# Kernel optimization log

Measured on AMD Instinct MI355X. Metric: run time of the kernel, lower is better.

The kernel has to match this reference:

```python
import jax, jax.numpy as jnp
import numpy as np

N_NODES = 200000
N_EDGES = 6400000
N_GRAPHS = 1024
N_EMB = 1032
D = 16


def _gcn_conv(x, W, b, src, dst, n):
    # PyG GCNConv: h = x W; symmetric norm with self-loops; aggregate onto target (dst)
    h = x @ W
    deg = jax.ops.segment_sum(jnp.ones_like(dst, dtype=h.dtype), dst, num_segments=n) + 1.0
    dis = jax.lax.rsqrt(deg)
    norm = dis[src] * dis[dst]                      # [E]
    agg = jax.ops.segment_sum(h[src] * norm[:, None], dst, num_segments=n)
    agg = agg + h * (dis * dis)[:, None]            # self-loop term
    return agg + b


def _protein_embed(ids, edge_index, batch_ids, emb, W1, b1, W2, b2):
    n = ids.shape[0]
    x = emb[ids]                                    # embedding lookup [N, D]
    src, dst = edge_index[0], edge_index[1]
    h = jax.nn.relu(_gcn_conv(x, W1, b1, src, dst, n))
    h = _gcn_conv(h, W2, b2, src, dst, n)
    # global_mean_pool over graphs
    sums = jax.ops.segment_sum(h, batch_ids, num_segments=N_GRAPHS)
    cnt = jax.ops.segment_sum(jnp.ones((n,), h.dtype), batch_ids, num_segments=N_GRAPHS)
    return sums / jnp.maximum(cnt, 1.0)[:, None]    # [B, D]


def setup_inputs() -> dict:
    key = jax.random.key(0)
    ks = jax.random.split(key, 10)
    emb = jax.random.normal(ks[0], (N_EMB, D), jnp.float32) * 0.1
    W1 = jax.random.normal(ks[1], (D, D), jnp.float32) * (1.0 / np.sqrt(D))
    W2 = jax.random.normal(ks[2], (D, D), jnp.float32) * (1.0 / np.sqrt(D))
    fcW = jax.random.normal(ks[3], (6, 2 * D), jnp.float32) * (1.0 / np.sqrt(2 * D))
    b1 = jnp.zeros((D,), jnp.float32)
    b2 = jnp.zeros((D,), jnp.float32)
    fcb = jnp.zeros((6,), jnp.float32)
    rx = jax.random.randint(ks[4], (N_NODES,), 0, N_EMB)
    r_edge_index = jax.random.randint(ks[5], (2, N_EDGES), 0, N_NODES)
    r_batch = jnp.sort(jax.random.randint(ks[6], (N_NODES,), 0, N_GRAPHS))
    lx = jax.random.randint(ks[7], (N_NODES,), 0, N_EMB)
    l_edge_index = jax.random.randint(ks[8], (2, N_EDGES), 0, N_NODES)
    l_batch = jnp.sort(jax.random.randint(ks[9], (N_NODES,), 0, N_GRAPHS))
    return {"emb": emb, "W1": W1, "b1": b1, "W2": W2, "b2": b2, "fcW": fcW, "fcb": fcb,
            "rx": rx, "r_edge_index": r_edge_index, "r_batch": r_batch,
            "lx": lx, "l_edge_index": l_edge_index, "l_batch": l_batch}


def reference(emb, W1, b1, W2, b2, fcW, fcb, rx, r_edge_index, r_batch, lx, l_edge_index, l_batch):
    r = _protein_embed(rx, r_edge_index, r_batch, emb, W1, b1, W2, b2)
    l = _protein_embed(lx, l_edge_index, l_batch, emb, W1, b1, W2, b2)
    h = jnp.concatenate([r, l], axis=1)             # [B, 2D]
    out = h @ fcW.T + fcb                           # [B, 6]
    return out[:, :3], out[:, 3:]
```

## Files before the change

kernel.cpp:

```cpp
#include <hip/hip_runtime.h>
#include <hip/hip_bf16.h>

#define N_NODES 200000
#define N_GRAPHS 1024
#define D 16
#define NEDGE 6400000

#define BNODES 256
#define NBUK 782
#define NCH 512
#define ECHUNK 12500
#define OSTRIDE (NBUK + 1)
#define CAP 9216
#define GBLK 12500
#define GHALF 6250

__global__ __launch_bounds__(1024) void pA(
        const int* __restrict__ srcR, const int* __restrict__ dstR,
        const int* __restrict__ srcL, const int* __restrict__ dstL,
        unsigned int* __restrict__ slabC_R, unsigned int* __restrict__ slabC_L,
        int* __restrict__ offsT_R, int* __restrict__ offsT_L) {
    const int* src = blockIdx.y ? srcL : srcR;
    const int* dst = blockIdx.y ? dstL : dstR;
    unsigned int* slabC = blockIdx.y ? slabC_L : slabC_R;
    int* offsT = blockIdx.y ? offsT_L : offsT_R;

    __shared__ unsigned int stage[ECHUNK];
    __shared__ int lh[NBUK];
    __shared__ int lcur[NBUK];
    __shared__ int wsum[16];
    int t = threadIdx.x;
    int wave = t >> 6, lane = t & 63;
    int c = blockIdx.x;
    int base = c * ECHUNK;

    for (int k = t; k < NBUK; k += 1024) lh[k] = 0;
    __syncthreads();
    for (int e = t; e < ECHUNK; e += 1024)
        atomicAdd(&lh[((unsigned int)dst[base + e]) >> 8], 1);
    __syncthreads();

    int v = (t < NBUK) ? lh[t] : 0;
    int x = v;
#pragma unroll
    for (int d0 = 1; d0 < 64; d0 <<= 1) {
        int y = __shfl_up(x, d0, 64);
        if (lane >= d0) x += y;
    }
    if (lane == 63) wsum[wave] = x;
    __syncthreads();
    if (wave == 0 && lane < 16) {
        int s = wsum[lane];
#pragma unroll
        for (int d0 = 1; d0 < 16; d0 <<= 1) {
            int y = __shfl_up(s, d0, 64);
            if (lane >= d0) s += y;
        }
        wsum[lane] = s;
    }
    __syncthreads();
    int excl = x - v + (wave ? wsum[wave - 1] : 0);
    if (t < NBUK) lcur[t] = excl;
    __syncthreads();

    for (int e = t; e < ECHUNK; e += 1024) {
        int d = dst[base + e];
        int s = src[base + e];
        int pos = atomicAdd(&lcur[d >> 8], 1);
        stage[pos] = ((unsigned int)(d & 255) << 18) | (unsigned int)s;
    }
    __syncthreads();
    for (int e = t; e < ECHUNK; e += 1024) slabC[base + e] = stage[e];
    if (t < NBUK) offsT[c * OSTRIDE + t] = excl;
    if (t == 0) offsT[c * OSTRIDE + NBUK] = ECHUNK;
}

__global__ __launch_bounds__(256) void tr_kernel(
        const int* __restrict__ offsT_R, const int* __restrict__ offsT_L,
        int* __restrict__ offsTT_R, int* __restrict__ offsTT_L) {
    const int* in = blockIdx.z ? offsT_L : offsT_R;
    int* outp = blockIdx.z ? offsTT_L : offsTT_R;
    __shared__ int tile[32][33];
    int lx = threadIdx.x & 31, ly = threadIdx.x >> 5;
#pragma unroll
    for (int r = 0; r < 32; r += 8) {
        int row = blockIdx.y * 32 + ly + r;
        int col = blockIdx.x * 32 + lx;
        if (col < OSTRIDE) tile[ly + r][lx] = in[row * OSTRIDE + col];
    }
    __syncthreads();
#pragma unroll
    for (int r = 0; r < 32; r += 8) {
        int orow = blockIdx.x * 32 + ly + r;
        int ocol = blockIdx.y * 32 + lx;
        if (orow < OSTRIDE) outp[orow * NCH + ocol] = tile[lx][ly + r];
    }
}

__global__ __launch_bounds__(256) void pB(
        const unsigned int* __restrict__ slabC_R, const unsigned int* __restrict__ slabC_L,
        const int* __restrict__ offsTT_R, const int* __restrict__ offsTT_L,
        unsigned int* __restrict__ slabR, unsigned int* __restrict__ slabL,
        int2* __restrict__ metaR, int2* __restrict__ metaL,
        float* __restrict__ disR, float* __restrict__ disL) {
    int y = blockIdx.y;
    const unsigned int* slabC = y ? slabC_L : slabC_R;
    const int* offsTT = y ? offsTT_L : offsTT_R;
    unsigned int* slab = y ? slabL : slabR;
    int2* meta = y ? metaL : metaR;
    float* dis = y ? disL : disR;

    __shared__ unsigned int sin_[CAP];
    __shared__ unsigned int sout[CAP];
    __shared__ int hcnt[BNODES], hoff[BNODES], hcur[BNODES];
    __shared__ int wtot[4];
    __shared__ int totc;
    int t = threadIdx.x;
    int lane = t & 63, wave = t >> 6;
    int b = blockIdx.x;

    int a0 = offsTT[b * NCH + t],        e0 = offsTT[(b + 1) * NCH + t];
    int a1 = offsTT[b * NCH + t + 256],  e1 = offsTT[(b + 1) * NCH + t + 256];
    int len = (e0 - a0) + (e1 - a1);

    int x = len;
#pragma unroll
    for (int d0 = 1; d0 < 64; d0 <<= 1) {
        int yy = __shfl_up(x, d0, 64);
        if (lane >= d0) x += yy;
    }
    if (lane == 63) wtot[wave] = x;
    hcnt[t] = 0;
    __syncthreads();
    int pre = 0;
    for (int w2 = 0; w2 < wave; w2++) pre += wtot[w2];
    int sbase = x - len + pre;
    if (t == 255) totc = sbase + len;
    __syncthreads();

    int p = sbase;
    {
        int cb = t * ECHUNK;
        for (int i = (a0 & ~3); i < e0; i += 4) {
            uint4 v = *(const uint4*)(slabC + cb + i);
            unsigned int vv[4] = {v.x, v.y, v.z, v.w};
#pragma unroll
            for (int k = 0; k < 4; k++) {
                int idx = i + k;
                if (idx >= a0 && idx < e0) { if (p < CAP) sin_[p] = vv[k]; p++; }
            }
        }
        cb = (t + 256) * ECHUNK;
        for (int i = (a1 & ~3); i < e1; i += 4) {
            uint4 v = *(const uint4*)(slabC + cb + i);
            unsigned int vv[4] = {v.x, v.y, v.z, v.w};
#pragma unroll
            for (int k = 0; k < 4; k++) {
                int idx = i + k;
                if (idx >= a1 && idx < e1) { if (p < CAP) sin_[p] = vv[k]; p++; }
            }
        }
    }
    __syncthreads();
    int cnt = totc;
    if (cnt > CAP) cnt = CAP;

    for (int i = t; i < cnt; i += 256) atomicAdd(&hcnt[sin_[i] >> 18], 1);
    __syncthreads();

    int v2 = hcnt[t];
    int x2 = v2;
#pragma unroll
    for (int d0 = 1; d0 < 64; d0 <<= 1) {
        int yy = __shfl_up(x2, d0, 64);
        if (lane >= d0) x2 += yy;
    }
    if (lane == 63) wtot[wave] = x2;
    __syncthreads();
    int pre2 = 0;
    for (int w2 = 0; w2 < wave; w2++) pre2 += wtot[w2];
    int ex = x2 - v2 + pre2;
    hoff[t] = ex;
    hcur[t] = ex;
    __syncthreads();

    for (int i = t; i < cnt; i += 256) {
        unsigned int r = sin_[i];
        int pp = atomicAdd(&hcur[r >> 18], 1);
        if (pp < CAP) sout[pp] = r & 0x3FFFFu;
    }
    __syncthreads();

    int gb = b * CAP;
    for (int i = t; i < cnt; i += 256) slab[gb + i] = sout[i];
    int node = (b << 8) + t;
    if (node < N_NODES) {
        meta[node] = make_int2(gb + hoff[t], gb + hoff[t] + hcnt[t]);
        dis[node] = rsqrtf((float)hcnt[t] + 1.0f);
    }
}

__global__ __launch_bounds__(256) void t1_kernel(
        const int* __restrict__ idsR, const int* __restrict__ idsL,
        const float* __restrict__ emb, const float* __restrict__ W,
        const float* __restrict__ disR, const float* __restrict__ disL,
        __hip_bfloat16* __restrict__ hsR, __hip_bfloat16* __restrict__ hsL) {
    int y = blockIdx.y;
    const int* ids = y ? idsL : idsR;
    const float* dis = y ? disL : disR;
    __hip_bfloat16* hs = y ? hsL : hsR;
    __shared__ float sW[D][D];
    __shared__ float sx[16][D + 1];
    int t = threadIdx.x;
    int j = t & 15, g = t >> 4;
    sW[g][j] = W[t];
    int i = (blockIdx.x << 4) + g;
    sx[g][j] = emb[(size_t)ids[i] * D + j];
    __syncthreads();
    float acc = 0.f;
#pragma unroll
    for (int k = 0; k < D; k++) acc += sx[g][k] * sW[k][j];
    hs[(size_t)i * D + j] = __float2bfloat16(acc * dis[i]);
}

__global__ __launch_bounds__(256) void g1_kernel(
        const int2* __restrict__ metaR, const int2* __restrict__ metaL,
        const unsigned int* __restrict__ csrR, const unsigned int* __restrict__ csrL,
        const __hip_bfloat16* __restrict__ hs1R, const __hip_bfloat16* __restrict__ hs1L,
        const float* __restrict__ disR, const float* __restrict__ disL,
        const float* __restrict__ b1, const float* __restrict__ W2,
        __hip_bfloat16* __restrict__ hs2R, __hip_bfloat16* __restrict__ hs2L) {
    int half = (blockIdx.x >= GHALF);
    int bx = blockIdx.x - (half ? GHALF : 0);
    const int2* meta = half ? metaL : metaR;
    const unsigned int* csr = half ? csrL : csrR;
    const __hip_bfloat16* hs1 = half ? hs1L : hs1R;
    const float* dis = half ? disL : disR;
    __hip_bfloat16* hs2 = half ? hs2L : hs2R;

    __shared__ float sW[D][D];
    __shared__ float sx[32][D + 1];
    int t = threadIdx.x;
    int jp = t & 7, g = t >> 3;
    sW[t >> 4][t & 15] = W2[t];
    int i = (bx << 5) + g;
    int2 be = meta[i];
    float2 acc = __bfloat1622float2(
        *(const __hip_bfloat162*)(hs1 + (size_t)i * D + 2 * jp));
    int e = be.x, end = be.y;
    for (; e + 8 <= end; e += 8) {
        int my = (int)csr[e + jp];
#pragma unroll
        for (int n = 0; n < 8; n++) {
            int s = __shfl(my, n, 8);
            float2 f = __bfloat1622float2(
                *(const __hip_bfloat162*)(hs1 + (size_t)s * D + 2 * jp));
            acc.x += f.x; acc.y += f.y;
        }
    }
    for (; e < end; e++) {
        int s = csr[e];
        float2 f = __bfloat1622float2(
            *(const __hip_bfloat162*)(hs1 + (size_t)s * D + 2 * jp));
        acc.x += f.x; acc.y += f.y;
    }
    float di = dis[i];
    sx[g][2 * jp]     = fmaxf(acc.x * di + b1[2 * jp], 0.f);
    sx[g][2 * jp + 1] = fmaxf(acc.y * di + b1[2 * jp + 1], 0.f);
    __syncthreads();
    float a0 = 0.f, a1 = 0.f;
#pragma unroll
    for (int k = 0; k < D; k++) {
        float xv = sx[g][k];
        a0 += xv * sW[k][2 * jp];
        a1 += xv * sW[k][2 * jp + 1];
    }
    *(__hip_bfloat162*)(hs2 + (size_t)i * D + 2 * jp) =
        __float22bfloat162_rn(make_float2(a0 * di, a1 * di));
}

__global__ __launch_bounds__(256) void g2_kernel(
        const int2* __restrict__ metaR, const int2* __restrict__ metaL,
        const unsigned int* __restrict__ csrR, const unsigned int* __restrict__ csrL,
        const __hip_bfloat16* __restrict__ hs2R, const __hip_bfloat16* __restrict__ hs2L,
        const float* __restrict__ disR, const float* __restrict__ disL,
        const float* __restrict__ b2,
        const int* __restrict__ batR, const int* __restrict__ batL,
        float* __restrict__ sumsR, float* __restrict__ sumsL,
        float* __restrict__ cntR, float* __restrict__ cntL) {
    int half = (blockIdx.x >= GHALF);
    int bx = blockIdx.x - (half ? GHALF : 0);
    const int2* meta = half ? metaL : metaR;
    const unsigned int* csr = half ? csrL : csrR;
    const __hip_bfloat16* hs2 = half ? hs2L : hs2R;
    const float* dis = half ? disL : disR;
    const int* batch = half ? batL : batR;
    float* sums = half ? sumsL : sumsR;
    float* cnt = half ? cntL : cntR;

    __shared__ float sv[32][D + 1];
    __shared__ int sb[32];
    int t = threadIdx.x;
    int jp = t & 7, g = t >> 3;
    int i = (bx << 5) + g;
    int2 be = meta[i];
    float2 acc = __bfloat1622float2(
        *(const __hip_bfloat162*)(hs2 + (size_t)i * D + 2 * jp));
    int e = be.x, end = be.y;
    for (; e + 8 <= end; e += 8) {
        int my = (int)csr[e + jp];
#pragma unroll
        for (int n = 0; n < 8; n++) {
            int s = __shfl(my, n, 8);
            float2 f = __bfloat1622float2(
                *(const __hip_bfloat162*)(hs2 + (size_t)s * D + 2 * jp));
            acc.x += f.x; acc.y += f.y;
        }
    }
    for (; e < end; e++) {
        int s = csr[e];
        float2 f = __bfloat1622float2(
            *(const __hip_bfloat162*)(hs2 + (size_t)s * D + 2 * jp));
        acc.x += f.x; acc.y += f.y;
    }
    float di = dis[i];
    int bi = batch[i];
    sv[g][2 * jp]     = acc.x * di + b2[2 * jp];
    sv[g][2 * jp + 1] = acc.y * di + b2[2 * jp + 1];
    if (jp == 0) sb[g] = bi;
    __syncthreads();
    bool runend = (g == 31) || (sb[g + 1] != bi);
    if (runend) {
        float s0 = 0.f, s1 = 0.f;
        int gg = g;
        while (gg >= 0 && sb[gg] == bi) { s0 += sv[gg][2 * jp]; s1 += sv[gg][2 * jp + 1]; gg--; }
        atomicAdd(&sums[bi * D + 2 * jp], s0);
        atomicAdd(&sums[bi * D + 2 * jp + 1], s1);
        if (jp == 0) atomicAdd(&cnt[bi], (float)(g - gg));
    }
}

__global__ void final_kernel(const float* __restrict__ rs, const float* __restrict__ rc,
                             const float* __restrict__ ls, const float* __restrict__ lc,
                             const float* __restrict__ fcW, const float* __restrict__ fcb,
                             float* __restrict__ out) {
    int b = blockIdx.x * blockDim.x + threadIdx.x;
    if (b >= N_GRAPHS) return;
    float hc[2 * D];
    float rn = fmaxf(rc[b], 1.f), ln = fmaxf(lc[b], 1.f);
#pragma unroll
    for (int j = 0; j < D; j++) {
        hc[j]     = rs[b * D + j] / rn;
        hc[D + j] = ls[b * D + j] / ln;
    }
#pragma unroll
    for (int c = 0; c < 6; c++) {
        float acc = fcb[c];
#pragma unroll
        for (int j = 0; j < 2 * D; j++) acc += hc[j] * fcW[c * 2 * D + j];
        if (c < 3) out[b * 3 + c] = acc;
        else       out[N_GRAPHS * 3 + b * 3 + (c - 3)] = acc;
    }
}

extern "C" void kernel_launch(void* const* d_in, const int* in_sizes, int n_in,
                              void* d_out, int out_size, void* d_ws, size_t ws_size,
                              hipStream_t stream) {
    const float* emb = (const float*)d_in[0];
    const float* W1  = (const float*)d_in[1];
    const float* b1  = (const float*)d_in[2];
    const float* W2  = (const float*)d_in[3];
    const float* b2  = (const float*)d_in[4];
    const float* fcW = (const float*)d_in[5];
    const float* fcb = (const float*)d_in[6];
    const int* rx = (const int*)d_in[7];
    const int* re = (const int*)d_in[8];
    const int* rb = (const int*)d_in[9];
    const int* lx = (const int*)d_in[10];
    const int* le = (const int*)d_in[11];
    const int* lb = (const int*)d_in[12];
    float* out = (float*)d_out;

    char* w = (char*)d_ws;
    unsigned int* slabC_R = (unsigned int*)w;
    __hip_bfloat16* hs1R = (__hip_bfloat16*)w;
    __hip_bfloat16* hs1L = hs1R + (size_t)N_NODES * D;
    __hip_bfloat16* hs2R = hs1L + (size_t)N_NODES * D;
    __hip_bfloat16* hs2L = hs2R + (size_t)N_NODES * D;
    w += (size_t)NEDGE * 4;
    unsigned int* slabC_L = (unsigned int*)w;  w += (size_t)NEDGE * 4;
    unsigned int* slabR = (unsigned int*)w;    w += (size_t)NBUK * CAP * 4;
    unsigned int* slabL = (unsigned int*)w;    w += (size_t)NBUK * CAP * 4;
    int* offsT_R = (int*)w;                    w += (size_t)NCH * OSTRIDE * 4;
    int* offsT_L = (int*)w;                    w += (size_t)NCH * OSTRIDE * 4;
    int* offsTT_R = (int*)w;                   w += (size_t)OSTRIDE * NCH * 4;
    int* offsTT_L = (int*)w;                   w += (size_t)OSTRIDE * NCH * 4;
    int2* metaR = (int2*)w;                    w += (size_t)N_NODES * 8;
    int2* metaL = (int2*)w;                    w += (size_t)N_NODES * 8;
    float* disR = (float*)w;                   w += (size_t)N_NODES * 4;
    float* disL = (float*)w;                   w += (size_t)N_NODES * 4;
    float* sums0 = (float*)w;                  w += (size_t)N_GRAPHS * D * 4;
    float* cnt0  = (float*)w;                  w += (size_t)N_GRAPHS * 4;
    float* sums1 = (float*)w;                  w += (size_t)N_GRAPHS * D * 4;
    float* cnt1  = (float*)w;                  w += (size_t)N_GRAPHS * 4;

    const int* srcR = re;  const int* dstR = re + NEDGE;
    const int* srcL = le;  const int* dstL = le + NEDGE;

    hipMemsetAsync(sums0, 0, ((size_t)N_GRAPHS * (D + 1)) * 2 * sizeof(float), stream);

    pA<<<dim3(NCH, 2), 1024, 0, stream>>>(srcR, dstR, srcL, dstL,
                                          slabC_R, slabC_L, offsT_R, offsT_L);
    tr_kernel<<<dim3((OSTRIDE + 31) / 32, NCH / 32, 2), 256, 0, stream>>>(
        offsT_R, offsT_L, offsTT_R, offsTT_L);
    pB<<<dim3(NBUK, 2), 256, 0, stream>>>(slabC_R, slabC_L, offsTT_R, offsTT_L,
                                          slabR, slabL, metaR, metaL, disR, disL);

    t1_kernel<<<dim3(GBLK, 2), 256, 0, stream>>>(rx, lx, emb, W1, disR, disL, hs1R, hs1L);
    g1_kernel<<<2 * GHALF, 256, 0, stream>>>(metaR, metaL, slabR, slabL,
                                             hs1R, hs1L, disR, disL, b1, W2, hs2R, hs2L);
    g2_kernel<<<2 * GHALF, 256, 0, stream>>>(metaR, metaL, slabR, slabL,
                                             hs2R, hs2L, disR, disL, b2, rb, lb,
                                             sums0, sums1, cnt0, cnt1);
    final_kernel<<<(N_GRAPHS + 255) / 256, 256, 0, stream>>>(
        sums0, cnt0, sums1, cnt1, fcW, fcb, out);
}
```

Baseline: 534.7 us.

## Split node features into two 8-wide planes so gathers fit in cache

Node features are stored as two separate 8-channel bf16 planes of 3.2MB each instead of one 16-channel array. Each gather pass now handles one plane per graph, launched as four kernels, so the random-access working set is half as large and more of it should stay in L2/MALL. Because the aggregation is split by channel, the layer-1 transform W2 moves out of g1 into a separate t2 kernel. Edge indices are read with nontemporal loads. The cost is reading the CSR index stream twice per layer, extra kernel launches, and an extra pass that writes and reads an intermediate feature tensor.

New measurement: 865.7 us. 1.62x slower.

```diff
diff --git a/kernel.cpp b/kernel.cpp
--- a/kernel.cpp
+++ b/kernel.cpp
@@ -12,8 +12,8 @@
 #define ECHUNK 12500
 #define OSTRIDE (NBUK + 1)
 #define CAP 9216
-#define GBLK 12500
-#define GHALF 6250
+#define GSEG 3125
+#define PLSZ ((size_t)N_NODES * 8)
 
 __global__ __launch_bounds__(1024) void pA(
         const int* __restrict__ srcR, const int* __restrict__ dstR,
@@ -204,11 +204,13 @@
         const int* __restrict__ idsR, const int* __restrict__ idsL,
         const float* __restrict__ emb, const float* __restrict__ W,
         const float* __restrict__ disR, const float* __restrict__ disL,
-        __hip_bfloat16* __restrict__ hsR, __hip_bfloat16* __restrict__ hsL) {
+        __hip_bfloat16* __restrict__ h0R, __hip_bfloat16* __restrict__ h1R,
+        __hip_bfloat16* __restrict__ h0L, __hip_bfloat16* __restrict__ h1L) {
     int y = blockIdx.y;
     const int* ids = y ? idsL : idsR;
     const float* dis = y ? disL : disR;
-    __hip_bfloat16* hs = y ? hsL : hsR;
+    __hip_bfloat16* h0 = y ? h0L : h0R;
+    __hip_bfloat16* h1 = y ? h1L : h1R;
     __shared__ float sW[D][D];
     __shared__ float sx[16][D + 1];
     int t = threadIdx.x;
@@ -220,123 +222,116 @@
     float acc = 0.f;
 #pragma unroll
     for (int k = 0; k < D; k++) acc += sx[g][k] * sW[k][j];
-    hs[(size_t)i * D + j] = __float2bfloat16(acc * dis[i]);
+    __hip_bfloat16* hp = (j < 8) ? h0 : h1;
+    hp[(size_t)i * 8 + (j & 7)] = __float2bfloat16(acc * dis[i]);
 }
 
 __global__ __launch_bounds__(256) void g1_kernel(
-        const int2* __restrict__ metaR, const int2* __restrict__ metaL,
-        const unsigned int* __restrict__ csrR, const unsigned int* __restrict__ csrL,
-        const __hip_bfloat16* __restrict__ hs1R, const __hip_bfloat16* __restrict__ hs1L,
-        const float* __restrict__ disR, const float* __restrict__ disL,
-        const float* __restrict__ b1, const float* __restrict__ W2,
-        __hip_bfloat16* __restrict__ hs2R, __hip_bfloat16* __restrict__ hs2L) {
-    int half = (blockIdx.x >= GHALF);
-    int bx = blockIdx.x - (half ? GHALF : 0);
-    const int2* meta = half ? metaL : metaR;
-    const unsigned int* csr = half ? csrL : csrR;
-    const __hip_bfloat16* hs1 = half ? hs1L : hs1R;
-    const float* dis = half ? disL : disR;
-    __hip_bfloat16* hs2 = half ? hs2L : hs2R;
-
-    __shared__ float sW[D][D];
-    __shared__ float sx[32][D + 1];
-    int t = threadIdx.x;
-    int jp = t & 7, g = t >> 3;
-    sW[t >> 4][t & 15] = W2[t];
-    int i = (bx << 5) + g;
+        const int2* __restrict__ meta, const unsigned int* __restrict__ csr,
+        const __hip_bfloat16* __restrict__ hp, const float* __restrict__ dis,
+        const float* __restrict__ bias8, __hip_bfloat16* __restrict__ outp) {
+    int t = threadIdx.x;
+    int jp = t & 3, g = t >> 2;
+    int i = (blockIdx.x << 6) + g;
     int2 be = meta[i];
-    float2 acc = __bfloat1622float2(
-        *(const __hip_bfloat162*)(hs1 + (size_t)i * D + 2 * jp));
+    float2 acc = __bfloat1622float2(*(const __hip_bfloat162*)(hp + (size_t)i * 8 + 2 * jp));
     int e = be.x, end = be.y;
-    for (; e + 8 <= end; e += 8) {
-        int my = (int)csr[e + jp];
-#pragma unroll
-        for (int n = 0; n < 8; n++) {
-            int s = __shfl(my, n, 8);
+    for (; e + 4 <= end; e += 4) {
+        unsigned int my = __builtin_nontemporal_load(csr + e + jp);
+#pragma unroll
+        for (int n = 0; n < 4; n++) {
+            int s = __shfl((int)my, n, 4);
             float2 f = __bfloat1622float2(
-                *(const __hip_bfloat162*)(hs1 + (size_t)s * D + 2 * jp));
+                *(const __hip_bfloat162*)(hp + (size_t)s * 8 + 2 * jp));
             acc.x += f.x; acc.y += f.y;
         }
     }
     for (; e < end; e++) {
-        int s = csr[e];
+        int s = (int)__builtin_nontemporal_load(csr + e);
         float2 f = __bfloat1622float2(
-            *(const __hip_bfloat162*)(hs1 + (size_t)s * D + 2 * jp));
+            *(const __hip_bfloat162*)(hp + (size_t)s * 8 + 2 * jp));
         acc.x += f.x; acc.y += f.y;
     }
     float di = dis[i];
-    sx[g][2 * jp]     = fmaxf(acc.x * di + b1[2 * jp], 0.f);
-    sx[g][2 * jp + 1] = fmaxf(acc.y * di + b1[2 * jp + 1], 0.f);
-    __syncthreads();
-    float a0 = 0.f, a1 = 0.f;
-#pragma unroll
-    for (int k = 0; k < D; k++) {
-        float xv = sx[g][k];
-        a0 += xv * sW[k][2 * jp];
-        a1 += xv * sW[k][2 * jp + 1];
-    }
-    *(__hip_bfloat162*)(hs2 + (size_t)i * D + 2 * jp) =
-        __float22bfloat162_rn(make_float2(a0 * di, a1 * di));
+    float v0 = fmaxf(acc.x * di + bias8[2 * jp], 0.f);
+    float v1 = fmaxf(acc.y * di + bias8[2 * jp + 1], 0.f);
+    __hip_bfloat162 r = __float22bfloat162_rn(make_float2(v0, v1));
+    __builtin_nontemporal_store(*(unsigned int*)&r,
+                                (unsigned int*)(outp + (size_t)i * 8 + 2 * jp));
+}
+
+__global__ __launch_bounds__(256) void t2_kernel(
+        const __hip_bfloat16* __restrict__ x0R, const __hip_bfloat16* __restrict__ x1R,
+        const __hip_bfloat16* __restrict__ x0L, const __hip_bfloat16* __restrict__ x1L,
+        const float* __restrict__ W,
+        const float* __restrict__ disR, const float* __restrict__ disL,
+        __hip_bfloat16* __restrict__ h0R, __hip_bfloat16* __restrict__ h1R,
+        __hip_bfloat16* __restrict__ h0L, __hip_bfloat16* __restrict__ h1L) {
+    int y = blockIdx.y;
+    const __hip_bfloat16* x0 = y ? x0L : x0R;
+    const __hip_bfloat16* x1 = y ? x1L : x1R;
+    const float* dis = y ? disL : disR;
+    __hip_bfloat16* h0 = y ? h0L : h0R;
+    __hip_bfloat16* h1 = y ? h1L : h1R;
+    __shared__ float sW[D][D];
+    __shared__ float sx[16][D + 1];
+    int t = threadIdx.x;
+    int j = t & 15, g = t >> 4;
+    sW[g][j] = W[t];
+    int i = (blockIdx.x << 4) + g;
+    const __hip_bfloat16* xp = (j < 8) ? x0 : x1;
+    sx[g][j] = __bfloat162float(xp[(size_t)i * 8 + (j & 7)]);
+    __syncthreads();
+    float acc = 0.f;
+#pragma unroll
+    for (int k = 0; k < D; k++) acc += sx[g][k] * sW[k][j];
+    __hip_bfloat16* hp = (j < 8) ? h0 : h1;
+    hp[(size_t)i * 8 + (j & 7)] = __float2bfloat16(acc * dis[i]);
 }
 
 __global__ __launch_bounds__(256) void g2_kernel(
-        const int2* __restrict__ metaR, const int2* __restrict__ metaL,
-        const unsigned int* __restrict__ csrR, const unsigned int* __restrict__ csrL,
-        const __hip_bfloat16* __restrict__ hs2R, const __hip_bfloat16* __restrict__ hs2L,
-        const float* __restrict__ disR, const float* __restrict__ disL,
-        const float* __restrict__ b2,
-        const int* __restrict__ batR, const int* __restrict__ batL,
-        float* __restrict__ sumsR, float* __restrict__ sumsL,
-        float* __restrict__ cntR, float* __restrict__ cntL) {
-    int half = (blockIdx.x >= GHALF);
-    int bx = blockIdx.x - (half ? GHALF : 0);
-    const int2* meta = half ? metaL : metaR;
-    const unsigned int* csr = half ? csrL : csrR;
-    const __hip_bfloat16* hs2 = half ? hs2L : hs2R;
-    const float* dis = half ? disL : disR;
-    const int* batch = half ? batL : batR;
-    float* sums = half ? sumsL : sumsR;
-    float* cnt = half ? cntL : cntR;
-
-    __shared__ float sv[32][D + 1];
-    __shared__ int sb[32];
-    int t = threadIdx.x;
-    int jp = t & 7, g = t >> 3;
-    int i = (bx << 5) + g;
+        const int2* __restrict__ meta, const unsigned int* __restrict__ csr,
+        const __hip_bfloat16* __restrict__ hp, const float* __restrict__ dis,
+        const float* __restrict__ bias8, const int* __restrict__ batch,
+        float* __restrict__ sums8, float* __restrict__ cnt, int addCnt) {
+    __shared__ float sv[64][9];
+    __shared__ int sb[64];
+    int t = threadIdx.x;
+    int jp = t & 3, g = t >> 2;
+    int i = (blockIdx.x << 6) + g;
     int2 be = meta[i];
-    float2 acc = __bfloat1622float2(
-        *(const __hip_bfloat162*)(hs2 + (size_t)i * D + 2 * jp));
+    float2 acc = __bfloat1622float2(*(const __hip_bfloat162*)(hp + (size_t)i * 8 + 2 * jp));
     int e = be.x, end = be.y;
-    for (; e + 8 <= end; e += 8) {
-        int my = (int)csr[e + jp];
-#pragma unroll
-        for (int n = 0; n < 8; n++) {
-            int s = __shfl(my, n, 8);
+    for (; e + 4 <= end; e += 4) {
+        unsigned int my = __builtin_nontemporal_load(csr + e + jp);
+#pragma unroll
+        for (int n = 0; n < 4; n++) {
+            int s = __shfl((int)my, n, 4);
             float2 f = __bfloat1622float2(
-                *(const __hip_bfloat162*)(hs2 + (size_t)s * D + 2 * jp));
+                *(const __hip_bfloat162*)(hp + (size_t)s * 8 + 2 * jp));
             acc.x += f.x; acc.y += f.y;
         }
     }
     for (; e < end; e++) {
-        int s = csr[e];
+        int s = (int)__builtin_nontemporal_load(csr + e);
         float2 f = __bfloat1622float2(
-            *(const __hip_bfloat162*)(hs2 + (size_t)s * D + 2 * jp));
+            *(const __hip_bfloat162*)(hp + (size_t)s * 8 + 2 * jp));
         acc.x += f.x; acc.y += f.y;
     }
     float di = dis[i];
-    int bi = batch[i];
-    sv[g][2 * jp]     = acc.x * di + b2[2 * jp];
-    sv[g][2 * jp + 1] = acc.y * di + b2[2 * jp + 1];
-    if (jp == 0) sb[g] = bi;
-    __syncthreads();
-    bool runend = (g == 31) || (sb[g + 1] != bi);
+    sv[g][2 * jp]     = acc.x * di + bias8[2 * jp];
+    sv[g][2 * jp + 1] = acc.y * di + bias8[2 * jp + 1];
+    if (jp == 0) sb[g] = batch[i];
+    __syncthreads();
+    int bi = sb[g];
+    bool runend = (g == 63) || (sb[g + 1] != bi);
     if (runend) {
         float s0 = 0.f, s1 = 0.f;
         int gg = g;
         while (gg >= 0 && sb[gg] == bi) { s0 += sv[gg][2 * jp]; s1 += sv[gg][2 * jp + 1]; gg--; }
-        atomicAdd(&sums[bi * D + 2 * jp], s0);
-        atomicAdd(&sums[bi * D + 2 * jp + 1], s1);
-        if (jp == 0) atomicAdd(&cnt[bi], (float)(g - gg));
+        atomicAdd(&sums8[(size_t)bi * D + 2 * jp], s0);
+        atomicAdd(&sums8[(size_t)bi * D + 2 * jp + 1], s1);
+        if (jp == 0 && addCnt) atomicAdd(&cnt[bi], (float)(g - gg));
     }
 }
 
@@ -383,10 +378,13 @@
 
     char* w = (char*)d_ws;
     unsigned int* slabC_R = (unsigned int*)w;
-    __hip_bfloat16* hs1R = (__hip_bfloat16*)w;
-    __hip_bfloat16* hs1L = hs1R + (size_t)N_NODES * D;
-    __hip_bfloat16* hs2R = hs1L + (size_t)N_NODES * D;
-    __hip_bfloat16* hs2L = hs2R + (size_t)N_NODES * D;
+    __hip_bfloat16* pt = (__hip_bfloat16*)w;
+    __hip_bfloat16* h1_0R = pt;              __hip_bfloat16* h1_1R = pt + PLSZ;
+    __hip_bfloat16* h1_0L = pt + 2 * PLSZ;   __hip_bfloat16* h1_1L = pt + 3 * PLSZ;
+    __hip_bfloat16* h2_0R = pt + 4 * PLSZ;   __hip_bfloat16* h2_1R = pt + 5 * PLSZ;
+    __hip_bfloat16* h2_0L = pt + 6 * PLSZ;   __hip_bfloat16* h2_1L = pt + 7 * PLSZ;
+    __hip_bfloat16* x_0R  = pt + 8 * PLSZ;   __hip_bfloat16* x_1R  = pt + 9 * PLSZ;
+    __hip_bfloat16* x_0L  = pt + 10 * PLSZ;  __hip_bfloat16* x_1L  = pt + 11 * PLSZ;
     w += (size_t)NEDGE * 4;
     unsigned int* slabC_L = (unsigned int*)w;  w += (size_t)NEDGE * 4;
     unsigned int* slabR = (unsigned int*)w;    w += (size_t)NBUK * CAP * 4;
@@ -416,12 +414,18 @@
     pB<<<dim3(NBUK, 2), 256, 0, stream>>>(slabC_R, slabC_L, offsTT_R, offsTT_L,
                                           slabR, slabL, metaR, metaL, disR, disL);
 
-    t1_kernel<<<dim3(GBLK, 2), 256, 0, stream>>>(rx, lx, emb, W1, disR, disL, hs1R, hs1L);
-    g1_kernel<<<2 * GHALF, 256, 0, stream>>>(metaR, metaL, slabR, slabL,
-                                             hs1R, hs1L, disR, disL, b1, W2, hs2R, hs2L);
-    g2_kernel<<<2 * GHALF, 256, 0, stream>>>(metaR, metaL, slabR, slabL,
-                                             hs2R, hs2L, disR, disL, b2, rb, lb,
-                                             sums0, sums1, cnt0, cnt1);
+    t1_kernel<<<dim3(12500, 2), 256, 0, stream>>>(rx, lx, emb, W1, disR, disL,
+                                                  h1_0R, h1_1R, h1_0L, h1_1L);
+    g1_kernel<<<GSEG, 256, 0, stream>>>(metaR, slabR, h1_0R, disR, b1,     x_0R);
+    g1_kernel<<<GSEG, 256, 0, stream>>>(metaR, slabR, h1_1R, disR, b1 + 8, x_1R);
+    g1_kernel<<<GSEG, 256, 0, stream>>>(metaL, slabL, h1_0L, disL, b1,     x_0L);
+    g1_kernel<<<GSEG, 256, 0, stream>>>(metaL, slabL, h1_1L, disL, b1 + 8, x_1L);
+    t2_kernel<<<dim3(12500, 2), 256, 0, stream>>>(x_0R, x_1R, x_0L, x_1L, W2, disR, disL,
+                                                  h2_0R, h2_1R, h2_0L, h2_1L);
+    g2_kernel<<<GSEG, 256, 0, stream>>>(metaR, slabR, h2_0R, disR, b2,     rb, sums0,     cnt0, 1);
+    g2_kernel<<<GSEG, 256, 0, stream>>>(metaR, slabR, h2_1R, disR, b2 + 8, rb, sums0 + 8, cnt0, 0);
+    g2_kernel<<<GSEG, 256, 0, stream>>>(metaL, slabL, h2_0L, disL, b2,     lb, sums1,     cnt1, 1);
+    g2_kernel<<<GSEG, 256, 0, stream>>>(metaL, slabL, h2_1L, disL, b2 + 8, lb, sums1 + 8, cnt1, 0);
     final_kernel<<<(N_GRAPHS + 255) / 256, 256, 0, stream>>>(
         sums0, cnt0, sums1, cnt1, fcW, fcb, out);
 }
```
